# Optimization experiments

Hardware: AMD Instinct MI355X
Metric: run time of the kernel (lower is better)

## Reference

```python
import jax, jax.numpy as jnp
import numpy as np

N = 100000
E = 1600000
IN_CH, HID_CH, OUT_CH, HEADS = 128, 32, 64, 4
NEG_SLOPE = 0.2


def gat_conv(x, src, dst, W, att_src, att_dst, bias, concat):
    """PyG-style GATConv (inference; dropout off). src/dst include self-loops.
    x: [N, Fin], W: [Fin, H*C], att_*: [H, C], bias: [H*C] or [C]."""
    n = x.shape[0]
    H, C = att_src.shape
    h = (x @ W).reshape(n, H, C)                      # [N, H, C]
    a_s = jnp.sum(h * att_src, axis=-1)               # [N, H]
    a_d = jnp.sum(h * att_dst, axis=-1)               # [N, H]
    e = jax.nn.leaky_relu(a_s[src] + a_d[dst], NEG_SLOPE)   # [E, H]
    # segment softmax over incoming edges of each dst node
    e_max = jax.ops.segment_max(e, dst, num_segments=n)     # [N, H]
    e_exp = jnp.exp(e - e_max[dst])                          # [E, H]
    denom = jax.ops.segment_sum(e_exp, dst, num_segments=n) # [N, H]
    alpha = e_exp / (denom[dst] + 1e-16)                     # [E, H]
    msg = h[src] * alpha[:, :, None]                         # [E, H, C]
    out = jax.ops.segment_sum(msg, dst, num_segments=n)     # [N, H, C]
    out = out.reshape(n, H * C) if concat else out.mean(axis=1)
    return out + bias


def setup_inputs() -> dict:
    key = jax.random.key(0)
    ks = jax.random.split(key, 10)
    g = 1.0 / np.sqrt(IN_CH)
    g2 = 1.0 / np.sqrt(HID_CH * HEADS)
    return {
        "x": jax.random.normal(ks[0], (N, IN_CH), dtype=jnp.float32),
        "edge_index": jax.random.randint(ks[1], (2, E), 0, N, dtype=jnp.int64),
        "W1": jax.random.normal(ks[2], (IN_CH, HEADS * HID_CH), dtype=jnp.float32) * g,
        "att_src1": jax.random.normal(ks[3], (HEADS, HID_CH), dtype=jnp.float32) * g,
        "att_dst1": jax.random.normal(ks[4], (HEADS, HID_CH), dtype=jnp.float32) * g,
        "b1": jnp.zeros((HEADS * HID_CH,), dtype=jnp.float32),
        "W2": jax.random.normal(ks[5], (HEADS * HID_CH, OUT_CH), dtype=jnp.float32) * g2,
        "att_src2": jax.random.normal(ks[6], (1, OUT_CH), dtype=jnp.float32) * g2,
        "att_dst2": jax.random.normal(ks[7], (1, OUT_CH), dtype=jnp.float32) * g2,
        "b2": jnp.zeros((OUT_CH,), dtype=jnp.float32),
    }


def reference(x, edge_index, W1, att_src1, att_dst1, b1, W2, att_src2, att_dst2, b2):
    n = x.shape[0]
    # GATConv adds self-loops by default (fixed-size concat: jit friendly)
    loops = jnp.arange(n, dtype=edge_index.dtype)
    src = jnp.concatenate([edge_index[0], loops])
    dst = jnp.concatenate([edge_index[1], loops])
    h = gat_conv(x, src, dst, W1, att_src1, att_dst1, b1, concat=True)
    h = jax.nn.elu(h)
    return gat_conv(h, src, dst, W2, att_src2, att_dst2, b2, concat=False)
```

## Files before the change

kernel.cpp:

```cpp
#include <hip/hip_runtime.h>
#include <hip/hip_fp16.h>

#define NEG_SLOPE 0.2f
#define BKN 128
#define MAXNB 1024
#define GRP 256

typedef _Float16 half_t;
typedef __attribute__((ext_vector_type(4))) _Float16 half4;
typedef __attribute__((ext_vector_type(8))) _Float16 half8;
typedef __attribute__((ext_vector_type(4))) float floatx4;

__device__ __forceinline__ float4 h4_to_f4(half4 h) {
    return make_float4((float)h[0], (float)h[1], (float)h[2], (float)h[3]);
}

__global__ __launch_bounds__(256) void w_convert2(
    const float* __restrict__ W1, half_t* __restrict__ Wt1,
    const float* __restrict__ W2, half_t* __restrict__ Wt2)
{
    int i = blockIdx.x * 256 + threadIdx.x;
    if (i < 128 * 128) {
        int k = i / 128, nn = i % 128;
        Wt1[nn * 128 + k] = (half_t)W1[i];
    } else if (i < 128 * 128 + 128 * 64) {
        int j = i - 128 * 128;
        int k = j / 64, nn = j % 64;
        Wt2[nn * 128 + k] = (half_t)W2[j];
    }
}

template<int BN, int HEADS>
__global__ __launch_bounds__(256) void gemm_mfma(
    const float* __restrict__ X, const half_t* __restrict__ Wt,
    const float* __restrict__ atts, const float* __restrict__ attd,
    half_t* __restrict__ H, float* __restrict__ As, float* __restrict__ Ad,
    int n)
{
    constexpr int K  = 128;
    constexpr int NT = BN / 16;
    constexpr int TPH = NT / HEADS;

    __shared__ half_t Wl[BN * K];
    __shared__ half_t Xl[64 * K];

    const int t = threadIdx.x;
    const int wave = t >> 6, lane = t & 63;
    const int quad = lane >> 4, c = lane & 15;

    float att_s[NT], att_d[NT];
    #pragma unroll
    for (int nt = 0; nt < NT; ++nt) {
        att_s[nt] = atts[nt * 16 + c];
        att_d[nt] = attd[nt * 16 + c];
    }

    for (int i = t; i < BN * 16; i += 256) {
        int row = i >> 4, cid = i & 15;
        half8 v = *(const half8*)(Wt + row * K + cid * 8);
        *(half8*)(Wl + row * K + ((cid ^ (row & 15)) << 3)) = v;
    }

    const int numTiles = (n + 63) / 64;
    for (int tile = blockIdx.x; tile < numTiles; tile += gridDim.x) {
        const int row0 = tile * 64;
        __syncthreads();
        for (int i = t; i < 1024; i += 256) {
            int m = i >> 4, cid = i & 15;
            int row = row0 + m;
            float4 a = make_float4(0.f,0.f,0.f,0.f), b = a;
            if (row < n) {
                const float4* src = (const float4*)(X + (size_t)row * K + cid * 8);
                a = src[0]; b = src[1];
            }
            half8 h;
            h[0]=(half_t)a.x; h[1]=(half_t)a.y; h[2]=(half_t)a.z; h[3]=(half_t)a.w;
            h[4]=(half_t)b.x; h[5]=(half_t)b.y; h[6]=(half_t)b.z; h[7]=(half_t)b.w;
            *(half8*)(Xl + m * K + ((cid ^ (m & 15)) << 3)) = h;
        }
        __syncthreads();

        floatx4 acc[NT];
        #pragma unroll
        for (int i = 0; i < NT; ++i) acc[i] = (floatx4)(0.f);

        #pragma unroll
        for (int kc = 0; kc < 4; ++kc) {
            int cid = kc * 4 + quad;
            half8 afrag = *(const half8*)(Xl + (wave * 16 + c) * K + ((cid ^ c) << 3));
            #pragma unroll
            for (int nt = 0; nt < NT; ++nt) {
                half8 bfrag = *(const half8*)(Wl + (nt * 16 + c) * K + ((cid ^ c) << 3));
                acc[nt] = __builtin_amdgcn_mfma_f32_16x16x32_f16(afrag, bfrag, acc[nt], 0, 0, 0);
            }
        }

        #pragma unroll
        for (int reg = 0; reg < 4; ++reg) {
            int row = row0 + wave * 16 + quad * 4 + reg;
            bool ok = row < n;
            if (ok) {
                #pragma unroll
                for (int nt = 0; nt < NT; ++nt)
                    H[(size_t)row * BN + nt * 16 + c] = (half_t)acc[nt][reg];
            }
            #pragma unroll
            for (int h = 0; h < HEADS; ++h) {
                float ps = 0.f, pd = 0.f;
                #pragma unroll
                for (int u = 0; u < TPH; ++u) {
                    int nt = h * TPH + u;
                    ps += acc[nt][reg] * att_s[nt];
                    pd += acc[nt][reg] * att_d[nt];
                }
                #pragma unroll
                for (int off = 1; off < 16; off <<= 1) {
                    ps += __shfl_xor(ps, off);
                    pd += __shfl_xor(pd, off);
                }
                if (ok && c == 0) {
                    As[(size_t)row * HEADS + h] = ps;
                    Ad[(size_t)row * HEADS + h] = pd;
                }
            }
        }
    }
}

__global__ __launch_bounds__(256) void ghist(
    const int* __restrict__ ei, int E, int Etot, int NB, int chunk,
    int* __restrict__ cnt)
{
    __shared__ int h[MAXNB];
    int g = blockIdx.x;
    for (int i = threadIdx.x; i < NB; i += 256) h[i] = 0;
    __syncthreads();
    int lo = g * chunk, hi = min(Etot, lo + chunk);
    for (int e = lo + threadIdx.x; e < hi; e += 256) {
        int dst = (e < E) ? ei[E + e] : (e - E);
        atomicAdd(&h[dst >> 7], 1);
    }
    __syncthreads();
    for (int i = threadIdx.x; i < NB; i += 256) cnt[i * GRP + g] = h[i];
}

__global__ __launch_bounds__(256) void scan_blocks(
    int* __restrict__ data, int n, int* __restrict__ bsum)
{
    __shared__ int s[256];
    int t = threadIdx.x;
    int idx = blockIdx.x * 1024 + t * 4;
    int4 v = make_int4(0, 0, 0, 0);
    if (idx + 3 < n)      v = *(const int4*)(data + idx);
    else {
        if (idx     < n) v.x = data[idx];
        if (idx + 1 < n) v.y = data[idx+1];
        if (idx + 2 < n) v.z = data[idx+2];
        if (idx + 3 < n) v.w = data[idx+3];
    }
    int tsum = v.x + v.y + v.z + v.w;
    s[t] = tsum;
    __syncthreads();
    for (int off = 1; off < 256; off <<= 1) {
        int x = (t >= off) ? s[t - off] : 0;
        __syncthreads();
        s[t] += x;
        __syncthreads();
    }
    int excl = s[t] - tsum;
    if (t == 255) bsum[blockIdx.x] = s[255];
    if (idx     < n) data[idx]     = excl;
    if (idx + 1 < n) data[idx + 1] = excl + v.x;
    if (idx + 2 < n) data[idx + 2] = excl + v.x + v.y;
    if (idx + 3 < n) data[idx + 3] = excl + v.x + v.y + v.z;
}

__global__ __launch_bounds__(256) void scan_sums(int* __restrict__ bsum, int nb)
{
    __shared__ int s[256];
    int t = threadIdx.x;
    int v = (t < nb) ? bsum[t] : 0;
    s[t] = v;
    __syncthreads();
    for (int off = 1; off < 256; off <<= 1) {
        int x = (t >= off) ? s[t - off] : 0;
        __syncthreads();
        s[t] += x;
        __syncthreads();
    }
    if (t < nb) bsum[t] = s[t] - v;
}

__global__ __launch_bounds__(256) void scan_add(
    int* __restrict__ data, int n, const int* __restrict__ bsum)
{
    int i = blockIdx.x * 256 + threadIdx.x;
    if (i < n) data[i] += bsum[i >> 10];
}

__global__ __launch_bounds__(256) void pass1_scatter(
    const int* __restrict__ ei, int E, int Etot, int NB, int chunk,
    const int* __restrict__ S, unsigned* __restrict__ tmp)
{
    __shared__ int cur[MAXNB];
    int g = blockIdx.x;
    for (int i = threadIdx.x; i < NB; i += 256) cur[i] = S[i * GRP + g];
    __syncthreads();
    int lo = g * chunk, hi = min(Etot, lo + chunk);
    for (int e = lo + threadIdx.x; e < hi; e += 256) {
        int src, dst;
        if (e < E) { src = ei[e]; dst = ei[E + e]; }
        else       { src = dst = e - E; }
        int pos = atomicAdd(&cur[dst >> 7], 1);
        tmp[pos] = ((unsigned)src << 7) | (unsigned)(dst & (BKN - 1));
    }
}

__global__ __launch_bounds__(256) void pass2_sort(
    const unsigned* __restrict__ tmp, const int* __restrict__ S,
    int NB, int Etot,
    int* __restrict__ offs, int* __restrict__ esrc, int n)
{
    __shared__ int cnt[BKN];
    __shared__ int sc[BKN];
    __shared__ int cur[BKN];
    int bk = blockIdx.x;
    int t  = threadIdx.x;
    if (t < BKN) cnt[t] = 0;
    __syncthreads();
    int lo = S[bk * GRP];
    int hi = (bk + 1 < NB) ? S[(bk + 1) * GRP] : Etot;
    for (int i = lo + t; i < hi; i += 256)
        atomicAdd(&cnt[tmp[i] & (BKN - 1)], 1);
    __syncthreads();
    int v = (t < BKN) ? cnt[t] : 0;
    if (t < BKN) sc[t] = v;
    __syncthreads();
    for (int off = 1; off < BKN; off <<= 1) {
        int x = (t < BKN && t >= off) ? sc[t - off] : 0;
        __syncthreads();
        if (t < BKN) sc[t] += x;
        __syncthreads();
    }
    if (t < BKN) {
        int node = bk * BKN + t;
        if (node < n) offs[node] = lo + sc[t];
        cur[t] = lo + sc[t] - v;
    }
    __syncthreads();
    for (int i = lo + t; i < hi; i += 256) {
        unsigned w = tmp[i];
        int p = atomicAdd(&cur[w & (BKN - 1)], 1);
        esrc[p] = (int)(w >> 7);
    }
}

__global__ __launch_bounds__(256) void agg1(
    const int* __restrict__ offs, const int* __restrict__ esrc,
    const half4* __restrict__ H4, const float* __restrict__ As,
    const float* __restrict__ Ad, const float* __restrict__ bias,
    float* __restrict__ X2, int n)
{
    int v    = (blockIdx.x * 256 + threadIdx.x) >> 6;
    int lane = threadIdx.x & 63;
    if (v >= n) return;
    int half = lane >> 5;
    int li   = lane & 31;
    int head = li >> 3;
    int end = offs[v];
    int beg = v ? offs[v - 1] : 0;
    float adv = Ad[(size_t)v * 4 + head];
    float a0 = 0.f, a1 = 0.f, a2 = 0.f, a3 = 0.f, den = 0.f;
    int j = beg + half;
    for (; j + 3 < end; j += 4) {
        int s0 = esrc[j], s1 = esrc[j + 2];
        float e0 = As[(size_t)s0 * 4 + head] + adv;
        float e1 = As[(size_t)s1 * 4 + head] + adv;
        half4 q0 = H4[(unsigned)s0 * 32 + li];
        half4 q1 = H4[(unsigned)s1 * 32 + li];
        e0 = e0 > 0.f ? e0 : NEG_SLOPE * e0;  float w0 = __expf(e0);
        e1 = e1 > 0.f ? e1 : NEG_SLOPE * e1;  float w1 = __expf(e1);
        float4 f0 = h4_to_f4(q0);
        float4 f1 = h4_to_f4(q1);
        a0 += w0 * f0.x + w1 * f1.x;
        a1 += w0 * f0.y + w1 * f1.y;
        a2 += w0 * f0.z + w1 * f1.z;
        a3 += w0 * f0.w + w1 * f1.w;
        den += w0 + w1;
    }
    for (; j < end; j += 2) {
        int s = esrc[j];
        float e = As[(size_t)s * 4 + head] + adv;
        e = e > 0.f ? e : NEG_SLOPE * e;
        float w = __expf(e);
        float4 f = h4_to_f4(H4[(unsigned)s * 32 + li]);
        a0 += w * f.x; a1 += w * f.y; a2 += w * f.z; a3 += w * f.w;
        den += w;
    }
    a0 += __shfl_xor(a0, 32);
    a1 += __shfl_xor(a1, 32);
    a2 += __shfl_xor(a2, 32);
    a3 += __shfl_xor(a3, 32);
    den += __shfl_xor(den, 32);
    if (half == 0) {
        float inv = 1.f / (den + 1e-16f);
        float4 b = ((const float4*)bias)[li];
        float o0 = a0 * inv + b.x, o1 = a1 * inv + b.y;
        float o2 = a2 * inv + b.z, o3 = a3 * inv + b.w;
        o0 = o0 > 0.f ? o0 : __expf(o0) - 1.f;
        o1 = o1 > 0.f ? o1 : __expf(o1) - 1.f;
        o2 = o2 > 0.f ? o2 : __expf(o2) - 1.f;
        o3 = o3 > 0.f ? o3 : __expf(o3) - 1.f;
        ((float4*)(X2 + (size_t)v * 128))[li] = make_float4(o0, o1, o2, o3);
    }
}

__global__ __launch_bounds__(256) void agg2(
    const int* __restrict__ offs, const int* __restrict__ esrc,
    const half4* __restrict__ H4, const float* __restrict__ As,
    const float* __restrict__ Ad, const float* __restrict__ bias,
    float* __restrict__ out, int n)
{
    int v    = (blockIdx.x * 256 + threadIdx.x) >> 6;
    int lane = threadIdx.x & 63;
    if (v >= n) return;
    int q  = lane >> 4;
    int li = lane & 15;
    int end = offs[v];
    int beg = v ? offs[v - 1] : 0;
    float adv = Ad[v];
    float a0 = 0.f, a1 = 0.f, a2 = 0.f, a3 = 0.f, den = 0.f;
    int j = beg + q;
    for (; j + 7 < end; j += 8) {
        int s0 = esrc[j], s1 = esrc[j + 4];
        float e0 = As[s0] + adv;
        float e1 = As[s1] + adv;
        half4 q0 = H4[(unsigned)s0 * 16 + li];
        half4 q1 = H4[(unsigned)s1 * 16 + li];
        e0 = e0 > 0.f ? e0 : NEG_SLOPE * e0;  float w0 = __expf(e0);
        e1 = e1 > 0.f ? e1 : NEG_SLOPE * e1;  float w1 = __expf(e1);
        float4 f0 = h4_to_f4(q0);
        float4 f1 = h4_to_f4(q1);
        a0 += w0 * f0.x + w1 * f1.x;
        a1 += w0 * f0.y + w1 * f1.y;
        a2 += w0 * f0.z + w1 * f1.z;
        a3 += w0 * f0.w + w1 * f1.w;
        den += w0 + w1;
    }
    for (; j < end; j += 4) {
        int s = esrc[j];
        float e = As[s] + adv;
        e = e > 0.f ? e : NEG_SLOPE * e;
        float w = __expf(e);
        float4 f = h4_to_f4(H4[(unsigned)s * 16 + li]);
        a0 += w * f.x; a1 += w * f.y; a2 += w * f.z; a3 += w * f.w;
        den += w;
    }
    #pragma unroll
    for (int off = 16; off <= 32; off <<= 1) {
        a0 += __shfl_xor(a0, off);
        a1 += __shfl_xor(a1, off);
        a2 += __shfl_xor(a2, off);
        a3 += __shfl_xor(a3, off);
        den += __shfl_xor(den, off);
    }
    if (lane < 16) {
        float inv = 1.f / (den + 1e-16f);
        float4 b = ((const float4*)bias)[li];
        ((float4*)(out + (size_t)v * 64))[li] =
            make_float4(a0 * inv + b.x, a1 * inv + b.y,
                        a2 * inv + b.z, a3 * inv + b.w);
    }
}

extern "C" void kernel_launch(void* const* d_in, const int* in_sizes, int n_in,
                              void* d_out, int out_size, void* d_ws, size_t ws_size,
                              hipStream_t stream)
{
    (void)n_in; (void)out_size; (void)ws_size;
    const float* x   = (const float*)d_in[0];
    const int*   ei  = (const int*)  d_in[1];
    const float* W1  = (const float*)d_in[2];
    const float* as1 = (const float*)d_in[3];
    const float* ad1 = (const float*)d_in[4];
    const float* b1  = (const float*)d_in[5];
    const float* W2  = (const float*)d_in[6];
    const float* as2 = (const float*)d_in[7];
    const float* ad2 = (const float*)d_in[8];
    const float* b2  = (const float*)d_in[9];
    float* out = (float*)d_out;

    const int n    = in_sizes[0] / 128;
    const int E    = in_sizes[1] / 2;
    const int Etot = E + n;
    const int NB   = (n + BKN - 1) / BKN;
    const int chunk = (Etot + GRP - 1) / GRP;

    char* p = (char*)d_ws;
    half_t* Hh = (half_t*)p;  p += (size_t)n * 128 * sizeof(half_t);
    float* X2  = (float*)p;   p += (size_t)n * 128 * sizeof(float);
    float* As1 = (float*)p;   p += (size_t)n * 4 * sizeof(float);
    float* Ad1 = (float*)p;   p += (size_t)n * 4 * sizeof(float);
    int* offs  = (int*)p;     p += (size_t)n * sizeof(int);
    int* esrc  = (int*)p;     p += (size_t)Etot * sizeof(int);
    unsigned* tmp = (unsigned*)p; p += (size_t)Etot * sizeof(unsigned);
    int* cnt   = (int*)p;     p += (size_t)NB * GRP * sizeof(int);
    int* bsum  = (int*)p;     p += 1024;
    half_t* Wt1 = (half_t*)p; p += 128 * 128 * sizeof(half_t);
    half_t* Wt2 = (half_t*)p; p += 64 * 128 * sizeof(half_t);

    const int scan_n  = NB * GRP;
    const int scan_nb = (scan_n + 1023) / 1024;

    w_convert2<<<(128 * 192 + 255) / 256, 256, 0, stream>>>(W1, Wt1, W2, Wt2);

    ghist<<<GRP, 256, 0, stream>>>(ei, E, Etot, NB, chunk, cnt);
    scan_blocks<<<scan_nb, 256, 0, stream>>>(cnt, scan_n, bsum);
    scan_sums<<<1, 256, 0, stream>>>(bsum, scan_nb);
    scan_add<<<(scan_n + 255) / 256, 256, 0, stream>>>(cnt, scan_n, bsum);
    pass1_scatter<<<GRP, 256, 0, stream>>>(ei, E, Etot, NB, chunk, cnt, tmp);
    pass2_sort<<<NB, 256, 0, stream>>>(tmp, cnt, NB, Etot, offs, esrc, n);

    const int gtiles = (n + 63) / 64;

    gemm_mfma<128, 4><<<gtiles, 256, 0, stream>>>(x, Wt1, as1, ad1, Hh, As1, Ad1, n);
    agg1<<<(n * 64 + 255) / 256, 256, 0, stream>>>(offs, esrc, (const half4*)Hh, As1, Ad1, b1, X2, n);

    gemm_mfma<64, 1><<<gtiles, 256, 0, stream>>>(X2, Wt2, as2, ad2, Hh, As1, Ad1, n);
    agg2<<<(n * 64 + 255) / 256, 256, 0, stream>>>(offs, esrc, (const half4*)Hh, As1, Ad1, b2, out, n);
}
```

Measured before the change: 338.6 us.

## Split H into per-32-column planes and aggregate each plane in separate passes

The GEMM epilogue now writes H as planes of 32 half columns (one plane per group of 32 features), and the aggregation runs one kernel launch per plane. Each pass gathers only 64 bytes per edge, so the randomly accessed working set per pass is smaller and may stay resident in L2/MALL. In exchange, the edge lists, the attention scalars and the per-edge exp are reloaded and recomputed for every pass (4x in layer 1, 2x in layer 2), and launch count grows.

```diff
diff --git a/kernel.cpp b/kernel.cpp
--- a/kernel.cpp
+++ b/kernel.cpp
@@ -7,13 +7,8 @@
 #define GRP 256
 
 typedef _Float16 half_t;
-typedef __attribute__((ext_vector_type(4))) _Float16 half4;
 typedef __attribute__((ext_vector_type(8))) _Float16 half8;
 typedef __attribute__((ext_vector_type(4))) float floatx4;
-
-__device__ __forceinline__ float4 h4_to_f4(half4 h) {
-    return make_float4((float)h[0], (float)h[1], (float)h[2], (float)h[3]);
-}
 
 __global__ __launch_bounds__(256) void w_convert2(
     const float* __restrict__ W1, half_t* __restrict__ Wt1,
@@ -101,8 +96,11 @@
             bool ok = row < n;
             if (ok) {
                 #pragma unroll
-                for (int nt = 0; nt < NT; ++nt)
-                    H[(size_t)row * BN + nt * 16 + c] = (half_t)acc[nt][reg];
+                for (int nt = 0; nt < NT; ++nt) {
+                    int g  = nt >> 1;
+                    int cf = ((nt & 1) << 4) + c;
+                    H[((size_t)g * n + row) * 32 + cf] = (half_t)acc[nt][reg];
+                }
             }
             #pragma unroll
             for (int h = 0; h < HEADS; ++h) {
@@ -255,71 +253,12 @@
     }
 }
 
-__global__ __launch_bounds__(256) void agg1(
+template<int HEADS, bool ELU>
+__global__ __launch_bounds__(256) void agg_pass(
     const int* __restrict__ offs, const int* __restrict__ esrc,
-    const half4* __restrict__ H4, const float* __restrict__ As,
-    const float* __restrict__ Ad, const float* __restrict__ bias,
-    float* __restrict__ X2, int n)
-{
-    int v    = (blockIdx.x * 256 + threadIdx.x) >> 6;
-    int lane = threadIdx.x & 63;
-    if (v >= n) return;
-    int half = lane >> 5;
-    int li   = lane & 31;
-    int head = li >> 3;
-    int end = offs[v];
-    int beg = v ? offs[v - 1] : 0;
-    float adv = Ad[(size_t)v * 4 + head];
-    float a0 = 0.f, a1 = 0.f, a2 = 0.f, a3 = 0.f, den = 0.f;
-    int j = beg + half;
-    for (; j + 3 < end; j += 4) {
-        int s0 = esrc[j], s1 = esrc[j + 2];
-        float e0 = As[(size_t)s0 * 4 + head] + adv;
-        float e1 = As[(size_t)s1 * 4 + head] + adv;
-        half4 q0 = H4[(unsigned)s0 * 32 + li];
-        half4 q1 = H4[(unsigned)s1 * 32 + li];
-        e0 = e0 > 0.f ? e0 : NEG_SLOPE * e0;  float w0 = __expf(e0);
-        e1 = e1 > 0.f ? e1 : NEG_SLOPE * e1;  float w1 = __expf(e1);
-        float4 f0 = h4_to_f4(q0);
-        float4 f1 = h4_to_f4(q1);
-        a0 += w0 * f0.x + w1 * f1.x;
-        a1 += w0 * f0.y + w1 * f1.y;
-        a2 += w0 * f0.z + w1 * f1.z;
-        a3 += w0 * f0.w + w1 * f1.w;
-        den += w0 + w1;
-    }
-    for (; j < end; j += 2) {
-        int s = esrc[j];
-        float e = As[(size_t)s * 4 + head] + adv;
-        e = e > 0.f ? e : NEG_SLOPE * e;
-        float w = __expf(e);
-        float4 f = h4_to_f4(H4[(unsigned)s * 32 + li]);
-        a0 += w * f.x; a1 += w * f.y; a2 += w * f.z; a3 += w * f.w;
-        den += w;
-    }
-    a0 += __shfl_xor(a0, 32);
-    a1 += __shfl_xor(a1, 32);
-    a2 += __shfl_xor(a2, 32);
-    a3 += __shfl_xor(a3, 32);
-    den += __shfl_xor(den, 32);
-    if (half == 0) {
-        float inv = 1.f / (den + 1e-16f);
-        float4 b = ((const float4*)bias)[li];
-        float o0 = a0 * inv + b.x, o1 = a1 * inv + b.y;
-        float o2 = a2 * inv + b.z, o3 = a3 * inv + b.w;
-        o0 = o0 > 0.f ? o0 : __expf(o0) - 1.f;
-        o1 = o1 > 0.f ? o1 : __expf(o1) - 1.f;
-        o2 = o2 > 0.f ? o2 : __expf(o2) - 1.f;
-        o3 = o3 > 0.f ? o3 : __expf(o3) - 1.f;
-        ((float4*)(X2 + (size_t)v * 128))[li] = make_float4(o0, o1, o2, o3);
-    }
-}
-
-__global__ __launch_bounds__(256) void agg2(
-    const int* __restrict__ offs, const int* __restrict__ esrc,
-    const half4* __restrict__ H4, const float* __restrict__ As,
-    const float* __restrict__ Ad, const float* __restrict__ bias,
-    float* __restrict__ out, int n)
+    const __half2* __restrict__ Hg, const float* __restrict__ As,
+    const float* __restrict__ Ad, const float* __restrict__ bias32,
+    float* __restrict__ Out, int n, int hh, int ldout, int colbase)
 {
     int v    = (blockIdx.x * 256 + threadIdx.x) >> 6;
     int lane = threadIdx.x & 63;
@@ -328,48 +267,46 @@
     int li = lane & 15;
     int end = offs[v];
     int beg = v ? offs[v - 1] : 0;
-    float adv = Ad[v];
-    float a0 = 0.f, a1 = 0.f, a2 = 0.f, a3 = 0.f, den = 0.f;
+    float adv = Ad[(size_t)v * HEADS + hh];
+    float ax = 0.f, ay = 0.f, den = 0.f;
     int j = beg + q;
     for (; j + 7 < end; j += 8) {
         int s0 = esrc[j], s1 = esrc[j + 4];
-        float e0 = As[s0] + adv;
-        float e1 = As[s1] + adv;
-        half4 q0 = H4[(unsigned)s0 * 16 + li];
-        half4 q1 = H4[(unsigned)s1 * 16 + li];
+        float e0 = As[(size_t)s0 * HEADS + hh] + adv;
+        float e1 = As[(size_t)s1 * HEADS + hh] + adv;
+        __half2 q0 = Hg[(size_t)s0 * 16 + li];
+        __half2 q1 = Hg[(size_t)s1 * 16 + li];
         e0 = e0 > 0.f ? e0 : NEG_SLOPE * e0;  float w0 = __expf(e0);
         e1 = e1 > 0.f ? e1 : NEG_SLOPE * e1;  float w1 = __expf(e1);
-        float4 f0 = h4_to_f4(q0);
-        float4 f1 = h4_to_f4(q1);
-        a0 += w0 * f0.x + w1 * f1.x;
-        a1 += w0 * f0.y + w1 * f1.y;
-        a2 += w0 * f0.z + w1 * f1.z;
-        a3 += w0 * f0.w + w1 * f1.w;
+        float2 f0 = __half22float2(q0);
+        float2 f1 = __half22float2(q1);
+        ax += w0 * f0.x + w1 * f1.x;
+        ay += w0 * f0.y + w1 * f1.y;
         den += w0 + w1;
     }
     for (; j < end; j += 4) {
         int s = esrc[j];
-        float e = As[s] + adv;
+        float e = As[(size_t)s * HEADS + hh] + adv;
         e = e > 0.f ? e : NEG_SLOPE * e;
         float w = __expf(e);
-        float4 f = h4_to_f4(H4[(unsigned)s * 16 + li]);
-        a0 += w * f.x; a1 += w * f.y; a2 += w * f.z; a3 += w * f.w;
-        den += w;
+        float2 f = __half22float2(Hg[(size_t)s * 16 + li]);
+        ax += w * f.x; ay += w * f.y; den += w;
     }
     #pragma unroll
     for (int off = 16; off <= 32; off <<= 1) {
-        a0 += __shfl_xor(a0, off);
-        a1 += __shfl_xor(a1, off);
-        a2 += __shfl_xor(a2, off);
-        a3 += __shfl_xor(a3, off);
+        ax += __shfl_xor(ax, off);
+        ay += __shfl_xor(ay, off);
         den += __shfl_xor(den, off);
     }
     if (lane < 16) {
         float inv = 1.f / (den + 1e-16f);
-        float4 b = ((const float4*)bias)[li];
-        ((float4*)(out + (size_t)v * 64))[li] =
-            make_float4(a0 * inv + b.x, a1 * inv + b.y,
-                        a2 * inv + b.z, a3 * inv + b.w);
+        float2 b = ((const float2*)bias32)[li];
+        float ox = ax * inv + b.x, oy = ay * inv + b.y;
+        if (ELU) {
+            ox = ox > 0.f ? ox : __expf(ox) - 1.f;
+            oy = oy > 0.f ? oy : __expf(oy) - 1.f;
+        }
+        ((float2*)(Out + (size_t)v * ldout + colbase))[li] = make_float2(ox, oy);
     }
 }
 
@@ -422,10 +359,17 @@
     pass2_sort<<<NB, 256, 0, stream>>>(tmp, cnt, NB, Etot, offs, esrc, n);
 
     const int gtiles = (n + 63) / 64;
+    const int ablocks = (n * 64 + 255) / 256;
 
     gemm_mfma<128, 4><<<gtiles, 256, 0, stream>>>(x, Wt1, as1, ad1, Hh, As1, Ad1, n);
-    agg1<<<(n * 64 + 255) / 256, 256, 0, stream>>>(offs, esrc, (const half4*)Hh, As1, Ad1, b1, X2, n);
+    for (int g = 0; g < 4; ++g)
+        agg_pass<4, true><<<ablocks, 256, 0, stream>>>(
+            offs, esrc, (const __half2*)(Hh + (size_t)g * n * 32),
+            As1, Ad1, b1 + g * 32, X2, n, g, 128, g * 32);
 
     gemm_mfma<64, 1><<<gtiles, 256, 0, stream>>>(X2, Wt2, as2, ad2, Hh, As1, Ad1, n);
-    agg2<<<(n * 64 + 255) / 256, 256, 0, stream>>>(offs, esrc, (const half4*)Hh, As1, Ad1, b2, out, n);
-}
+    for (int g = 0; g < 2; ++g)
+        agg_pass<1, false><<<ablocks, 256, 0, stream>>>(
+            offs, esrc, (const __half2*)(Hh + (size_t)g * n * 32),
+            As1, Ad1, b2 + g * 32, out, n, 0, 64, g * 32);
+}
```

Measured after the change: 512.7 us. +51.4%, slower.
